# Kernel tuning notes

Hardware: AMD Instinct MI355X
Metric: run time of the kernel (lower is better)

Reference implementation:

```python
import jax, jax.numpy as jnp
import numpy as np

BINS = 10          # config.bins
SCOPE = 2          # config.dropout_scope_lowest (continue_train=True)
BASE_RATE = 0.0    # self.dropout_rate = zeros(1) when continue_train
THRESH = (BINS - SCOPE) / BINS   # edges[bins - dropout_scope]
UPPER = 1.0 + 1e-6               # edges[bins] (last edge += 1e-6)


def _forward(pred, target, rand_mat, hard_rand, pos_prop):
    B, C = pred.shape
    Bf = jnp.asarray(B, pred.dtype)
    # BCEWithLogits, reduction='none': logaddexp(0,x) - x*t
    bce = jnp.logaddexp(0.0, pred) - pred * target                     # [B,C]
    # g is detached in the torch code
    g = jax.lax.stop_gradient(jnp.abs(jax.nn.sigmoid(pred) - target))  # [B,C]
    # per-class loss -> normalized -> per-class dropout rate
    loss_c = bce.sum(0)                                                # [C]
    ln = jnp.log10(1.0 + loss_c)
    norm = 5.0 - 10.0 * (ln - ln.min()) / (ln.max() - ln.min())
    drate = jnp.maximum(jax.nn.sigmoid(norm), BASE_RATE)               # [C]
    # pos/neg balance bookkeeping (all per-class)
    pos_sum = target.sum(0)                                            # [C]
    neg_sum = Bf - pos_sum
    bal_pos = pos_prop * Bf
    bal_neg = Bf - bal_pos
    pos_gt = pos_sum > bal_pos                                         # majority is positives
    neg_gt = neg_sum > bal_neg                                         # majority is negatives
    balance_num = jnp.where(pos_gt, bal_pos, jnp.where(neg_gt, bal_neg, 0.0))
    dropout_num = jnp.floor(
        jnp.where(pos_gt, pos_sum - bal_pos,
                  jnp.where(neg_gt, neg_sum - bal_neg, 0.0))).astype(jnp.int32)
    # hard/easy class split: uniform(1,C) > dropout_rate
    hard = hard_rand[0] > drate                                        # [C] bool
    maj_lab = pos_gt.astype(pred.dtype)
    min_lab = neg_gt.astype(pred.dtype)
    is_maj = target == maj_lab[None, :]                                # [B,C]
    is_min = target == min_lab[None, :]
    maj_cnt = is_maj.sum(0).astype(pred.dtype)                         # [C]
    min_cnt = is_min.sum(0).astype(pred.dtype)
    # hard branch: reweight majority samples to balance_num/|majority|
    w_hard = jnp.where(is_maj, (balance_num / jnp.maximum(maj_cnt, 1.0))[None, :], 1.0)
    # easy branch: zero the dropout_num easiest (smallest g) majority samples,
    # rescale minority by (B - balance_num)/|minority|
    g_m = jnp.where(is_maj, g, jnp.inf)
    ranks = jnp.argsort(jnp.argsort(g_m, axis=0), axis=0)              # rank among majority by g asc
    drop_easy = is_maj & (ranks < dropout_num[None, :])
    w_easy = jnp.where(is_min & (min_cnt > 0)[None, :],
                       ((Bf - balance_num) / jnp.maximum(min_cnt, 1.0))[None, :], 1.0)
    w_easy = jnp.where(drop_easy, 0.0, w_easy)
    weights = jnp.where(hard[None, :], w_hard, w_easy)                 # [B,C]
    # random dropping of high-|g| (hard-gradient band) samples
    idxs = ((g >= THRESH) & (g < UPPER)).astype(pred.dtype)
    drop_idxs = (rand_mat > drate[None, :]).astype(pred.dtype)
    weights = weights * (1.0 - drop_idxs * idxs)
    return (bce * weights).mean()


def setup_inputs() -> dict:
    key = jax.random.key(0)
    k1, k2, k3, k4, k5 = jax.random.split(key, 5)
    B, C = 131072, 40
    pred = jax.random.normal(k1, (B, C), jnp.float32) * 2.0
    target = jax.random.bernoulli(k2, 0.5, (B, C)).astype(jnp.float32)
    rand_mat = jax.random.uniform(k3, (B, C), jnp.float32)
    hard_rand = jax.random.uniform(k4, (1, C), jnp.float32)
    pos_prop = jax.random.uniform(k5, (C,), jnp.float32, minval=0.3, maxval=0.7)
    return {"pred": pred, "target": target, "rand_mat": rand_mat,
            "hard_rand": hard_rand, "pos_prop": pos_prop}


def reference(pred, target, rand_mat, hard_rand, pos_prop):
    return _forward(pred, target, rand_mat, hard_rand, pos_prop)
```

## Files before the change

### kernel.cpp

```cpp
#include <hip/hip_runtime.h>
#include <hip/hip_bf16.h>
#include <math.h>
#include <stddef.h>

#define BN 131072
#define CN 40
#define NTOT (BN * CN)
#define MASKW (BN / 64)
#define NBLK 1024
#define NCHUNK 8
#define CROWS (BN / NCHUNK)

struct Ws {
    double acc;
    double pad0;
    unsigned ghist0[CN][4096];
    unsigned ghist1[CN][1024];
    unsigned ghist2[CN][256];
    double lossc[CN];
    int    posc[CN];
    float drate[CN];
    float majl[CN];
    float minl[CN];
    float w_hard[CN];
    float w_easy[CN];
    int   hardf[CN];
    int   kdrop[CN];
    int   minpos[CN];
    union {
        unsigned long long mask[CN][MASKW];
        struct { float lpart[CN][NBLK]; int ppart[CN][NBLK]; } parts;
    } u;
    unsigned long long eqmask[CN][MASKW];
    unsigned keys[CN][BN];
};

__device__ __forceinline__ float bce_f(float x, float t) {
    float m = fmaxf(x, 0.0f);
    return m + log1pf(expf(-fabsf(x))) - x * t;
}
__device__ __forceinline__ float g_f(float x, float t) {
    float s = 1.0f / (1.0f + expf(-x));
    return fabsf(s - t);
}
__device__ __forceinline__ void bce_g(float x, float t, float& bce, float& g) {
    float e   = expf(-fabsf(x));
    bce       = fmaxf(x, 0.0f) + log1pf(e) - x * t;
    float inv = 1.0f / (1.0f + e);
    float s   = (x >= 0.0f) ? inv : e * inv;
    g         = fabsf(s - t);
}
__device__ __forceinline__ unsigned masked_key(unsigned key, unsigned majb) {
    return ((key & 1u) == majb) ? (key >> 1) : 0xFFFFFFFFu;
}
__device__ __forceinline__ bool col_active(const Ws* ws, int c) {
    return (ws->kdrop[c] > 0) && (ws->hardf[c] == 0);
}

template<int PER, int NBINS>
__device__ __forceinline__ void scan_pick(const unsigned* __restrict__ gh,
                                          unsigned krem,
                                          unsigned* wsum ,
                                          unsigned* out2 ) {
    int tid = threadIdx.x, lane = tid & 63, w = tid >> 6;
    unsigned v[PER];
    unsigned s = 0;
    #pragma unroll
    for (int i = 0; i < PER; ++i) {
        int idx = tid * PER + i;
        v[i] = (idx < NBINS) ? gh[idx] : 0u;
        s += v[i];
    }
    unsigned isc = s;
    #pragma unroll
    for (int d = 1; d < 64; d <<= 1) {
        unsigned o = __shfl_up(isc, (unsigned)d, 64);
        if (lane >= d) isc += o;
    }
    if (lane == 63) wsum[w] = isc;
    __syncthreads();
    unsigned wpre = 0;
    #pragma unroll
    for (int j = 0; j < 16; ++j) wpre += (j < w) ? wsum[j] : 0u;
    unsigned inc = wpre + isc, prev = inc - s;
    if (prev < krem && inc >= krem) {
        unsigned cum = prev;
        #pragma unroll
        for (int i = 0; i < PER; ++i) {
            if (cum < krem && cum + v[i] >= krem) {
                out2[0] = (unsigned)(tid * PER + i);
                out2[1] = krem - cum;
            }
            cum += v[i];
        }
    }
    __syncthreads();
}

__global__ __launch_bounds__(640) void k_fuse(const float* __restrict__ pred,
                                              const float* __restrict__ tgt,
                                              Ws* __restrict__ ws) {
    __shared__ unsigned shk[128 * 41];
    __shared__ float sl[CN];
    __shared__ int   sp[CN];
    int tid = threadIdx.x;
    if (tid < CN) { sl[tid] = 0.0f; sp[tid] = 0; }
    __syncthreads();

    int  tile  = (blockIdx.x & 7) * 128 + (blockIdx.x >> 3);
    long tile0 = (long)tile * 5120;
    int  c0    = (tid * 4) % 40;
    float accl[4] = {0, 0, 0, 0};
    int   cntp[4] = {0, 0, 0, 0};

    #pragma unroll
    for (int j = 0; j < 2; ++j) {
        int e = j * 2560 + tid * 4;
        const float4 p = *(const float4*)(pred + tile0 + e);
        const float4 t = *(const float4*)(tgt + tile0 + e);
        int r = e / 40;
        #pragma unroll
        for (int u = 0; u < 4; ++u) {
            float pu = (&p.x)[u], tu = (&t.x)[u];
            float bce, g;
            bce_g(pu, tu, bce, g);
            accl[u] += bce;
            int tb = (tu != 0.0f) ? 1 : 0;
            cntp[u] += tb;
            shk[r * 41 + c0 + u] = (__float_as_uint(g) << 1) | (unsigned)tb;
        }
    }
    #pragma unroll
    for (int u = 0; u < 4; ++u) {
        atomicAdd(&sl[c0 + u], accl[u]);
        atomicAdd(&sp[c0 + u], cntp[u]);
    }
    __syncthreads();

    int w = tid / 128, r = tid % 128;
    int row0 = tile * 128;
    #pragma unroll
    for (int cc = 0; cc < 8; ++cc) {
        int c = w * 8 + cc;
        ws->keys[c][row0 + r] = shk[r * 41 + c];
    }
    if (tid < CN) {
        ws->u.parts.lpart[tid][blockIdx.x] = sl[tid];
        ws->u.parts.ppart[tid][blockIdx.x] = sp[tid];
    }
}

__global__ __launch_bounds__(1024) void k_params(const float* __restrict__ hard_rand,
                                                 const float* __restrict__ pos_prop,
                                                 Ws* __restrict__ ws, int use_part) {
    int tid = threadIdx.x;
    __shared__ double sred[CN][17];
    __shared__ int    spre[CN][17];
    __shared__ double lossv[CN];
    __shared__ int    posv[CN];
    __shared__ double lns[CN];
    __shared__ double smn, smx;
    if (use_part) {
        if (tid < CN * 16) {
            int c = tid >> 4, j = tid & 15;
            double s = 0.0; int p = 0;
            for (int i = j; i < NBLK; i += 16) {
                s += (double)ws->u.parts.lpart[c][i];
                p += ws->u.parts.ppart[c][i];
            }
            sred[c][j] = s; spre[c][j] = p;
        }
        __syncthreads();
        if (tid < CN) {
            double s = 0.0; int p = 0;
            for (int j = 0; j < 16; ++j) { s += sred[tid][j]; p += spre[tid][j]; }
            lossv[tid] = s; posv[tid] = p;
        }
    } else {
        if (tid < CN) { lossv[tid] = ws->lossc[tid]; posv[tid] = ws->posc[tid]; }
    }
    __syncthreads();
    if (tid < CN) lns[tid] = log10(1.0 + lossv[tid]);
    __syncthreads();
    if (tid == 0) {
        double a = lns[0], b = lns[0];
        for (int i = 1; i < CN; i++) { a = fmin(a, lns[i]); b = fmax(b, lns[i]); }
        smn = a; smx = b;
    }
    __syncthreads();
    if (tid < CN) {
        int c = tid;
        double norm = 5.0 - 10.0 * (lns[c] - smn) / (smx - smn);
        float drate = (float)(1.0 / (1.0 + exp(-norm)));
        float Bf = (float)BN;
        float pos_sum = (float)posv[c];
        float neg_sum = Bf - pos_sum;
        float bal_pos = pos_prop[c] * Bf;
        float bal_neg = Bf - bal_pos;
        bool pos_gt = pos_sum > bal_pos;
        bool neg_gt = neg_sum > bal_neg;
        float balance = pos_gt ? bal_pos : (neg_gt ? bal_neg : 0.0f);
        float dnum_f  = pos_gt ? (pos_sum - bal_pos)
                               : (neg_gt ? (neg_sum - bal_neg) : 0.0f);
        int   kdrop   = (int)floorf(dnum_f);
        float majl = pos_gt ? 1.0f : 0.0f;
        float minl = neg_gt ? 1.0f : 0.0f;
        float maj_cnt = (majl == 1.0f) ? pos_sum : neg_sum;
        float min_cnt = (minl == 1.0f) ? pos_sum : neg_sum;
        ws->drate[c]  = drate;
        ws->majl[c]   = majl;
        ws->minl[c]   = minl;
        ws->w_hard[c] = balance / fmaxf(maj_cnt, 1.0f);
        ws->w_easy[c] = (Bf - balance) / fmaxf(min_cnt, 1.0f);
        ws->hardf[c]  = (hard_rand[c] > drate) ? 1 : 0;
        ws->kdrop[c]  = kdrop;
        ws->minpos[c] = (min_cnt > 0.0f) ? 1 : 0;
    }
}

__global__ __launch_bounds__(1024) void k_hist0(Ws* __restrict__ ws) {
    int c = blockIdx.x >> 3, chunk = blockIdx.x & 7;
    if (!col_active(ws, c)) return;
    unsigned majb = (ws->majl[c] != 0.0f) ? 1u : 0u;
    const uint4* __restrict__ kc4 =
        (const uint4*)(ws->keys[c] + chunk * CROWS);
    __shared__ unsigned h[4096];
    int tid = threadIdx.x;
    for (int i = tid; i < 4096; i += 1024) h[i] = 0;
    __syncthreads();
    for (int b4 = tid; b4 < CROWS / 4; b4 += 1024) {
        uint4 kk = kc4[b4];
        unsigned ks[4] = {kk.x, kk.y, kk.z, kk.w};
        #pragma unroll
        for (int q = 0; q < 4; ++q)
            if ((ks[q] & 1u) == majb) atomicAdd(&h[(ks[q] >> 1) >> 18], 1u);
    }
    __syncthreads();
    for (int i = tid; i < 4096; i += 1024)
        if (h[i]) atomicAdd(&ws->ghist0[c][i], h[i]);
}

__global__ __launch_bounds__(1024) void k_hist1(Ws* __restrict__ ws) {
    int c = blockIdx.x >> 3, chunk = blockIdx.x & 7;
    if (!col_active(ws, c)) return;
    __shared__ unsigned wsum[16];
    __shared__ unsigned out2[2];
    scan_pick<4, 4096>(ws->ghist0[c], (unsigned)ws->kdrop[c], wsum, out2);
    unsigned p0 = out2[0];
    unsigned majb = (ws->majl[c] != 0.0f) ? 1u : 0u;
    const uint4* __restrict__ kc4 =
        (const uint4*)(ws->keys[c] + chunk * CROWS);
    __shared__ unsigned h[1024];
    int tid = threadIdx.x;
    h[tid] = 0;
    __syncthreads();
    for (int b4 = tid; b4 < CROWS / 4; b4 += 1024) {
        uint4 kk = kc4[b4];
        unsigned ks[4] = {kk.x, kk.y, kk.z, kk.w};
        #pragma unroll
        for (int q = 0; q < 4; ++q)
            if ((ks[q] & 1u) == majb) {
                unsigned mk = ks[q] >> 1;
                if ((mk >> 18) == p0) atomicAdd(&h[(mk >> 8) & 0x3FFu], 1u);
            }
    }
    __syncthreads();
    if (h[tid]) atomicAdd(&ws->ghist1[c][tid], h[tid]);
}

__global__ __launch_bounds__(1024) void k_hist2(Ws* __restrict__ ws) {
    int c = blockIdx.x >> 3, chunk = blockIdx.x & 7;
    if (!col_active(ws, c)) return;
    __shared__ unsigned wsum[16];
    __shared__ unsigned out2[2];
    scan_pick<4, 4096>(ws->ghist0[c], (unsigned)ws->kdrop[c], wsum, out2);
    unsigned p0 = out2[0], krem1 = out2[1];
    scan_pick<1, 1024>(ws->ghist1[c], krem1, wsum, out2);
    unsigned pp = (p0 << 10) | out2[0];
    unsigned majb = (ws->majl[c] != 0.0f) ? 1u : 0u;
    const uint4* __restrict__ kc4 =
        (const uint4*)(ws->keys[c] + chunk * CROWS);
    __shared__ unsigned h[256];
    int tid = threadIdx.x;
    if (tid < 256) h[tid] = 0;
    __syncthreads();
    for (int b4 = tid; b4 < CROWS / 4; b4 += 1024) {
        uint4 kk = kc4[b4];
        unsigned ks[4] = {kk.x, kk.y, kk.z, kk.w};
        #pragma unroll
        for (int q = 0; q < 4; ++q)
            if ((ks[q] & 1u) == majb) {
                unsigned mk = ks[q] >> 1;
                if ((mk >> 8) == pp) atomicAdd(&h[mk & 0xFFu], 1u);
            }
    }
    __syncthreads();
    if (tid < 256 && h[tid]) atomicAdd(&ws->ghist2[c][tid], h[tid]);
}

__global__ __launch_bounds__(1024) void k_mask(Ws* __restrict__ ws) {
    int c = blockIdx.x >> 3, chunk = blockIdx.x & 7;
    int tid = threadIdx.x;
    unsigned long long* mrow = ws->u.mask[c];
    if (!col_active(ws, c)) {
        if (tid < MASKW / NCHUNK) mrow[chunk * (MASKW / NCHUNK) + tid] = 0ull;
        return;
    }
    __shared__ unsigned wsum[16];
    __shared__ unsigned out2[2];
    scan_pick<4, 4096>(ws->ghist0[c], (unsigned)ws->kdrop[c], wsum, out2);
    unsigned p0 = out2[0], krem1 = out2[1];
    scan_pick<1, 1024>(ws->ghist1[c], krem1, wsum, out2);
    unsigned p1 = out2[0], krem2 = out2[1];
    scan_pick<1, 256>(ws->ghist2[c], krem2, wsum, out2);
    unsigned T = (p0 << 18) | (p1 << 8) | out2[0];

    unsigned majb = (ws->majl[c] != 0.0f) ? 1u : 0u;
    const unsigned* __restrict__ kc = ws->keys[c];
    unsigned long long* erow = ws->eqmask[c];
    int lane = tid & 63, w = tid >> 6;
    int base = chunk * CROWS;
    for (int it = 0; it < CROWS / 1024; ++it) {
        int b = base + it * 1024 + tid;
        unsigned m = masked_key(kc[b], majb);
        unsigned long long blt = __ballot(m < T);
        unsigned long long beq = __ballot(m == T);
        if (lane == 0) {
            int word = (base >> 6) + it * 16 + w;
            mrow[word] = blt;
            erow[word] = beq;
        }
    }
}

__global__ __launch_bounds__(1024) void k_tie(Ws* __restrict__ ws) {
    int c = blockIdx.x;
    if (!col_active(ws, c)) return;
    __shared__ unsigned wsum[16];
    __shared__ unsigned out2[2];
    scan_pick<4, 4096>(ws->ghist0[c], (unsigned)ws->kdrop[c], wsum, out2);
    unsigned krem1 = out2[1];
    scan_pick<1, 1024>(ws->ghist1[c], krem1, wsum, out2);
    unsigned krem2 = out2[1];
    scan_pick<1, 256>(ws->ghist2[c], krem2, wsum, out2);
    unsigned need = out2[1];

    int tid = threadIdx.x, lane = tid & 63, w = tid >> 6;
    const unsigned long long* erow = ws->eqmask[c];
    unsigned long long* mrow = ws->u.mask[c];
    unsigned long long e0 = erow[2 * tid], e1 = erow[2 * tid + 1];
    unsigned pc0 = (unsigned)__popcll(e0), pc1 = (unsigned)__popcll(e1);
    unsigned cnt = pc0 + pc1;
    unsigned isc = cnt;
    #pragma unroll
    for (int d = 1; d < 64; d <<= 1) {
        unsigned o = __shfl_up(isc, (unsigned)d, 64);
        if (lane >= d) isc += o;
    }
    if (lane == 63) wsum[w] = isc;
    __syncthreads();
    unsigned wpre = 0;
    #pragma unroll
    for (int j = 0; j < 16; ++j) wpre += (j < w) ? wsum[j] : 0u;
    unsigned prev = wpre + isc - cnt;

    #pragma unroll
    for (int half = 0; half < 2; ++half) {
        unsigned long long e = half ? e1 : e0;
        unsigned pc = half ? pc1 : pc0;
        unsigned p  = half ? prev + pc0 : prev;
        if (pc > 0 && p < need) {
            unsigned keep = need - p;
            if (keep > pc) keep = pc;
            unsigned long long sel;
            if (keep == pc) sel = e;
            else {
                sel = 0ull;
                unsigned long long m = e;
                for (unsigned i = 0; i < keep; ++i) {
                    unsigned long long lsb = m & (~m + 1ull);
                    sel |= lsb;
                    m ^= lsb;
                }
            }
            mrow[2 * tid + half] |= sel;
        }
    }
}

__global__ __launch_bounds__(640) void k_final2(const float* __restrict__ pred,
                                                const float* __restrict__ tgt,
                                                const float* __restrict__ rnd,
                                                Ws* __restrict__ ws) {
    int tid = threadIdx.x;
    long tile0 = (long)blockIdx.x * 5120;
    int  c0    = (tid * 4) % 40;
    float drate[4], majl[4], minl[4], wh[4], we[4];
    int hf[4], mp[4];
    #pragma unroll
    for (int u = 0; u < 4; ++u) {
        int c = c0 + u;
        drate[u] = ws->drate[c]; majl[u] = ws->majl[c]; minl[u] = ws->minl[c];
        wh[u] = ws->w_hard[c];   we[u] = ws->w_easy[c];
        hf[u] = ws->hardf[c];    mp[u] = ws->minpos[c];
    }
    double acc = 0.0;
    #pragma unroll
    for (int j = 0; j < 2; ++j) {
        long i = tile0 + j * 2560 + tid * 4;
        const float4 p  = *(const float4*)(pred + i);
        const float4 t  = *(const float4*)(tgt + i);
        const float4 rr = *(const float4*)(rnd + i);
        int b = (int)(i / 40);
        int wsh = b >> 6, bit = b & 63;
        #pragma unroll
        for (int u = 0; u < 4; ++u) {
            float pu = (&p.x)[u], tu = (&t.x)[u], ru = (&rr.x)[u];
            float bce, g;
            bce_g(pu, tu, bce, g);
            float w;
            if (hf[u]) {
                w = (tu == majl[u]) ? wh[u] : 1.0f;
            } else {
                bool dropped = (ws->u.mask[c0 + u][wsh] >> bit) & 1ull;
                w = dropped ? 0.0f : ((tu == minl[u] && mp[u]) ? we[u] : 1.0f);
            }
            if (g >= 0.8f && g < 1.000001f && ru > drate[u]) w = 0.0f;
            acc += (double)(bce * w);
        }
    }
    __shared__ double sd[640];
    sd[tid] = acc;
    __syncthreads();
    for (int s = 320; s >= 5; s >>= 1) {
        if (tid < s) sd[tid] += sd[tid + s];
        __syncthreads();
    }
    if (tid == 0) {
        double v = sd[0] + sd[1] + sd[2] + sd[3] + sd[4];
        atomicAdd(&ws->acc, v);
    }
}

__global__ void k_write(Ws* __restrict__ ws, float* __restrict__ out) {
    out[0] = (float)(ws->acc / (double)NTOT);
}

__global__ void k_colreduce(const float* __restrict__ pred,
                            const float* __restrict__ tgt,
                            Ws* __restrict__ ws) {
    __shared__ float sl[CN];
    __shared__ int   sp[CN];
    int tid = threadIdx.x;
    if (tid < CN) { sl[tid] = 0.0f; sp[tid] = 0; }
    __syncthreads();
    int stride = gridDim.x * blockDim.x;
    for (int i = blockIdx.x * blockDim.x + tid; i < NTOT; i += stride) {
        int c = i % CN;
        float p = pred[i], t = tgt[i];
        atomicAdd(&sl[c], bce_f(p, t));
        if (t != 0.0f) atomicAdd(&sp[c], 1);
    }
    __syncthreads();
    if (tid < CN) {
        atomicAdd(&ws->lossc[tid], (double)sl[tid]);
        atomicAdd(&ws->posc[tid], sp[tid]);
    }
}

__global__ __launch_bounds__(1024) void k_select(const float* __restrict__ pred,
                                                 const float* __restrict__ tgt,
                                                 Ws* __restrict__ ws) {
    int c   = blockIdx.x;
    int tid = threadIdx.x;
    int k   = ws->kdrop[c];
    bool easy = (ws->hardf[c] == 0);
    unsigned long long* mrow = ws->u.mask[c];
    if (k <= 0 || !easy) {
        for (int i = tid; i < MASKW; i += 1024) mrow[i] = 0ull;
        return;
    }
    float majl = ws->majl[c];
    __shared__ unsigned h[256];
    __shared__ unsigned cum[256];
    __shared__ unsigned sh_sel, sh_krem;
    unsigned prefix = 0;
    unsigned krem   = (unsigned)k;
    for (int level = 0; level < 4; ++level) {
        int shift = 24 - 8 * level;
        for (int i = tid; i < 256; i += 1024) h[i] = 0;
        __syncthreads();
        for (int b = tid; b < BN; b += 1024) {
            float t = tgt[b * CN + c];
            if (t == majl) {
                unsigned bits = __float_as_uint(g_f(pred[b * CN + c], t));
                bool ok = (level == 0) || ((bits >> (shift + 8)) == prefix);
                if (ok) atomicAdd(&h[(bits >> shift) & 0xFFu], 1u);
            }
        }
        __syncthreads();
        if (tid < 256) cum[tid] = h[tid];
        __syncthreads();
        for (int off = 1; off < 256; off <<= 1) {
            unsigned v = 0;
            if (tid < 256 && tid >= off) v = cum[tid - off];
            __syncthreads();
            if (tid < 256 && tid >= off) cum[tid] += v;
            __syncthreads();
        }
        if (tid < 256) {
            unsigned prev = (tid == 0) ? 0u : cum[tid - 1];
            if (cum[tid] >= krem && prev < krem) {
                sh_sel  = (unsigned)tid;
                sh_krem = krem - prev;
            }
        }
        __syncthreads();
        prefix = (prefix << 8) | sh_sel;
        krem   = sh_krem;
        __syncthreads();
    }
    unsigned T    = prefix;
    unsigned need = krem;
    __shared__ unsigned wcnt[16];
    unsigned base = 0;
    int lane = tid & 63, wid = tid >> 6;
    for (int chunk = 0; chunk < BN / 1024; ++chunk) {
        int b = chunk * 1024 + tid;
        float t = tgt[b * CN + c];
        bool ismaj = (t == majl);
        unsigned bits = 0xFFFFFFFFu;
        if (ismaj) bits = __float_as_uint(g_f(pred[b * CN + c], t));
        bool lt = ismaj && (bits < T);
        bool eq = ismaj && (bits == T);
        unsigned long long bal = __ballot(eq);
        if (lane == 0) wcnt[wid] = (unsigned)__popcll(bal);
        __syncthreads();
        unsigned woff = 0, tot = 0;
        for (int w = 0; w < 16; ++w) {
            unsigned v = wcnt[w];
            if (w < wid) woff += v;
            tot += v;
        }
        unsigned long long lanemask = (lane == 0) ? 0ull : ((~0ull) >> (64 - lane));
        unsigned myrank = base + woff + (unsigned)__popcll(bal & lanemask);
        bool dropped = lt || (eq && myrank < need);
        unsigned long long bd = __ballot(dropped);
        if (lane == 0) mrow[chunk * 16 + wid] = bd;
        base += tot;
        __syncthreads();
    }
}

__global__ void k_final(const float* __restrict__ pred,
                        const float* __restrict__ tgt,
                        const float* __restrict__ rnd,
                        Ws* __restrict__ ws) {
    __shared__ double sdata[256];
    double acc = 0.0;
    int stride = gridDim.x * blockDim.x;
    for (int i = blockIdx.x * blockDim.x + threadIdx.x; i < NTOT; i += stride) {
        int b = i / CN;
        int c = i - b * CN;
        float p = pred[i], t = tgt[i], r = rnd[i];
        float bce = bce_f(p, t);
        float g   = g_f(p, t);
        float w;
        if (ws->hardf[c]) {
            w = (t == ws->majl[c]) ? ws->w_hard[c] : 1.0f;
        } else {
            bool dropped = (ws->u.mask[c][b >> 6] >> (b & 63)) & 1ull;
            if (dropped) w = 0.0f;
            else w = ((t == ws->minl[c]) && ws->minpos[c]) ? ws->w_easy[c] : 1.0f;
        }
        if ((g >= 0.8f) && (g < 1.000001f) && (r > ws->drate[c])) w = 0.0f;
        acc += (double)(bce * w);
    }
    sdata[threadIdx.x] = acc;
    __syncthreads();
    for (int s = blockDim.x / 2; s > 0; s >>= 1) {
        if (threadIdx.x < s) sdata[threadIdx.x] += sdata[threadIdx.x + s];
        __syncthreads();
    }
    if (threadIdx.x == 0) atomicAdd(&ws->acc, sdata[0]);
}

extern "C" void kernel_launch(void* const* d_in, const int* in_sizes, int n_in,
                              void* d_out, int out_size, void* d_ws, size_t ws_size,
                              hipStream_t stream) {
    const float* pred      = (const float*)d_in[0];
    const float* tgt       = (const float*)d_in[1];
    const float* rnd       = (const float*)d_in[2];
    const float* hard_rand = (const float*)d_in[3];
    const float* pos_prop  = (const float*)d_in[4];
    Ws* ws = (Ws*)d_ws;

    if (ws_size >= sizeof(Ws)) {
        hipMemsetAsync(d_ws, 0, offsetof(Ws, lossc), stream);
        k_fuse  <<<NBLK, 640, 0, stream>>>(pred, tgt, ws);
        k_params<<<1, 1024, 0, stream>>>(hard_rand, pos_prop, ws, 1);
        k_hist0 <<<CN * NCHUNK, 1024, 0, stream>>>(ws);
        k_hist1 <<<CN * NCHUNK, 1024, 0, stream>>>(ws);
        k_hist2 <<<CN * NCHUNK, 1024, 0, stream>>>(ws);
        k_mask  <<<CN * NCHUNK, 1024, 0, stream>>>(ws);
        k_tie   <<<CN, 1024, 0, stream>>>(ws);
        k_final2<<<NBLK, 640, 0, stream>>>(pred, tgt, rnd, ws);
    } else {
        hipMemsetAsync(d_ws, 0, offsetof(Ws, drate), stream);
        k_colreduce<<<2048, 256, 0, stream>>>(pred, tgt, ws);
        k_params<<<1, 1024, 0, stream>>>(hard_rand, pos_prop, ws, 0);
        k_select<<<CN, 1024, 0, stream>>>(pred, tgt, ws);
        k_final <<<2048, 256, 0, stream>>>(pred, tgt, rnd, ws);
    }
    k_write<<<1, 1, 0, stream>>>(ws, (float*)d_out);
}
```

Baseline: 209.2 us.

## Fuse param computation into first histogram pass and fold final write into reduce

```diff
diff --git a/kernel.cpp b/kernel.cpp
--- a/kernel.cpp
+++ b/kernel.cpp
@@ -13,7 +13,8 @@
 
 struct Ws {
     double acc;
-    double pad0;
+    unsigned done;
+    unsigned pad0;
     unsigned ghist0[CN][4096];
     unsigned ghist1[CN][1024];
     unsigned ghist2[CN][256];
@@ -36,17 +37,19 @@
 };
 
 __device__ __forceinline__ float bce_f(float x, float t) {
-    float m = fmaxf(x, 0.0f);
-    return m + log1pf(expf(-fabsf(x))) - x * t;
+    float e = __expf(-fabsf(x));
+    return fmaxf(x, 0.0f) + __logf(1.0f + e) - x * t;
 }
 __device__ __forceinline__ float g_f(float x, float t) {
-    float s = 1.0f / (1.0f + expf(-x));
+    float e   = __expf(-fabsf(x));
+    float inv = __builtin_amdgcn_rcpf(1.0f + e);
+    float s   = (x >= 0.0f) ? inv : e * inv;
     return fabsf(s - t);
 }
 __device__ __forceinline__ void bce_g(float x, float t, float& bce, float& g) {
-    float e   = expf(-fabsf(x));
-    bce       = fmaxf(x, 0.0f) + log1pf(e) - x * t;
-    float inv = 1.0f / (1.0f + e);
+    float e   = __expf(-fabsf(x));
+    bce       = fmaxf(x, 0.0f) + __logf(1.0f + e) - x * t;
+    float inv = __builtin_amdgcn_rcpf(1.0f + e);
     float s   = (x >= 0.0f) ? inv : e * inv;
     g         = fabsf(s - t);
 }
@@ -150,37 +153,324 @@
     }
 }
 
+__global__ __launch_bounds__(1024) void k_sel0(const float* __restrict__ hard_rand,
+                                               const float* __restrict__ pos_prop,
+                                               Ws* __restrict__ ws) {
+    const int bid = blockIdx.x;
+    const int c = bid >> 3, chunk = bid & 7;
+    const int tid = threadIdx.x, lane = tid & 63, wv = tid >> 6;
+
+    __shared__ unsigned h[4096];
+    __shared__ double s_lns[CN];
+    __shared__ int s_pos;
+    __shared__ int s_active, s_kdrop;
+    __shared__ unsigned s_majb;
+
+    for (int j = wv; j < CN; j += 16) {
+        double s = 0.0;
+        for (int q = lane; q < NBLK; q += 64)
+            s += (double)ws->u.parts.lpart[j][q];
+        #pragma unroll
+        for (int d = 32; d >= 1; d >>= 1) s += __shfl_down(s, d, 64);
+        if (lane == 0) s_lns[j] = log10(1.0 + s);
+    }
+    if (wv == 15) {
+        int p = 0;
+        for (int q = lane; q < NBLK; q += 64) p += ws->u.parts.ppart[c][q];
+        #pragma unroll
+        for (int d = 32; d >= 1; d >>= 1) p += __shfl_down(p, d, 64);
+        if (lane == 0) s_pos = p;
+    }
+    __syncthreads();
+    if (tid == 0) {
+        double mn = s_lns[0], mx = s_lns[0];
+        for (int i = 1; i < CN; ++i) { mn = fmin(mn, s_lns[i]); mx = fmax(mx, s_lns[i]); }
+        double norm = 5.0 - 10.0 * (s_lns[c] - mn) / (mx - mn);
+        float drate = (float)(1.0 / (1.0 + exp(-norm)));
+        float Bf = (float)BN;
+        float pos_sum = (float)s_pos;
+        float neg_sum = Bf - pos_sum;
+        float bal_pos = pos_prop[c] * Bf;
+        float bal_neg = Bf - bal_pos;
+        bool pos_gt = pos_sum > bal_pos;
+        bool neg_gt = neg_sum > bal_neg;
+        float balance = pos_gt ? bal_pos : (neg_gt ? bal_neg : 0.0f);
+        float dnum_f  = pos_gt ? (pos_sum - bal_pos)
+                               : (neg_gt ? (neg_sum - bal_neg) : 0.0f);
+        int   kdrop   = (int)floorf(dnum_f);
+        float majl = pos_gt ? 1.0f : 0.0f;
+        float minl = neg_gt ? 1.0f : 0.0f;
+        float maj_cnt = (majl == 1.0f) ? pos_sum : neg_sum;
+        float min_cnt = (minl == 1.0f) ? pos_sum : neg_sum;
+        int hardf = (hard_rand[c] > drate) ? 1 : 0;
+        if (chunk == 0) {
+            ws->drate[c]  = drate;
+            ws->majl[c]   = majl;
+            ws->minl[c]   = minl;
+            ws->w_hard[c] = balance / fmaxf(maj_cnt, 1.0f);
+            ws->w_easy[c] = (Bf - balance) / fmaxf(min_cnt, 1.0f);
+            ws->hardf[c]  = hardf;
+            ws->kdrop[c]  = kdrop;
+            ws->minpos[c] = (min_cnt > 0.0f) ? 1 : 0;
+        }
+        s_active = (kdrop > 0 && hardf == 0) ? 1 : 0;
+        s_kdrop  = kdrop;
+        s_majb   = (majl != 0.0f) ? 1u : 0u;
+    }
+    __syncthreads();
+    if (!s_active) return;
+    const unsigned majb = s_majb;
+    const uint4* kc4 = (const uint4*)(ws->keys[c] + chunk * CROWS);
+
+    for (int i = tid; i < 4096; i += 1024) h[i] = 0;
+    __syncthreads();
+    for (int b4 = tid; b4 < CROWS / 4; b4 += 1024) {
+        uint4 kk = kc4[b4];
+        unsigned ks[4] = {kk.x, kk.y, kk.z, kk.w};
+        #pragma unroll
+        for (int q = 0; q < 4; ++q)
+            if ((ks[q] & 1u) == majb) atomicAdd(&h[(ks[q] >> 1) >> 18], 1u);
+    }
+    __syncthreads();
+    for (int i = tid; i < 4096; i += 1024)
+        if (h[i]) atomicAdd(&ws->ghist0[c][i], h[i]);
+}
+
+__global__ __launch_bounds__(1024) void k_hist1(Ws* __restrict__ ws) {
+    int c = blockIdx.x >> 3, chunk = blockIdx.x & 7;
+    if (!col_active(ws, c)) return;
+    __shared__ unsigned wsum[16];
+    __shared__ unsigned out2[2];
+    scan_pick<4, 4096>(ws->ghist0[c], (unsigned)ws->kdrop[c], wsum, out2);
+    unsigned p0 = out2[0];
+    unsigned majb = (ws->majl[c] != 0.0f) ? 1u : 0u;
+    const uint4* __restrict__ kc4 = (const uint4*)(ws->keys[c] + chunk * CROWS);
+    __shared__ unsigned h[1024];
+    int tid = threadIdx.x;
+    h[tid] = 0;
+    __syncthreads();
+    for (int b4 = tid; b4 < CROWS / 4; b4 += 1024) {
+        uint4 kk = kc4[b4];
+        unsigned ks[4] = {kk.x, kk.y, kk.z, kk.w};
+        #pragma unroll
+        for (int q = 0; q < 4; ++q)
+            if ((ks[q] & 1u) == majb) {
+                unsigned mk = ks[q] >> 1;
+                if ((mk >> 18) == p0) atomicAdd(&h[(mk >> 8) & 0x3FFu], 1u);
+            }
+    }
+    __syncthreads();
+    if (h[tid]) atomicAdd(&ws->ghist1[c][tid], h[tid]);
+}
+
+__global__ __launch_bounds__(1024) void k_hist2(Ws* __restrict__ ws) {
+    int c = blockIdx.x >> 3, chunk = blockIdx.x & 7;
+    if (!col_active(ws, c)) return;
+    __shared__ unsigned wsum[16];
+    __shared__ unsigned out2[2];
+    scan_pick<4, 4096>(ws->ghist0[c], (unsigned)ws->kdrop[c], wsum, out2);
+    unsigned p0 = out2[0], krem1 = out2[1];
+    scan_pick<1, 1024>(ws->ghist1[c], krem1, wsum, out2);
+    unsigned pp = (p0 << 10) | out2[0];
+    unsigned majb = (ws->majl[c] != 0.0f) ? 1u : 0u;
+    const uint4* __restrict__ kc4 = (const uint4*)(ws->keys[c] + chunk * CROWS);
+    __shared__ unsigned h[256];
+    int tid = threadIdx.x;
+    if (tid < 256) h[tid] = 0;
+    __syncthreads();
+    for (int b4 = tid; b4 < CROWS / 4; b4 += 1024) {
+        uint4 kk = kc4[b4];
+        unsigned ks[4] = {kk.x, kk.y, kk.z, kk.w};
+        #pragma unroll
+        for (int q = 0; q < 4; ++q)
+            if ((ks[q] & 1u) == majb) {
+                unsigned mk = ks[q] >> 1;
+                if ((mk >> 8) == pp) atomicAdd(&h[mk & 0xFFu], 1u);
+            }
+    }
+    __syncthreads();
+    if (tid < 256 && h[tid]) atomicAdd(&ws->ghist2[c][tid], h[tid]);
+}
+
+__global__ __launch_bounds__(1024) void k_mask(Ws* __restrict__ ws) {
+    int c = blockIdx.x >> 3, chunk = blockIdx.x & 7;
+    int tid = threadIdx.x;
+    unsigned long long* mrow = ws->u.mask[c];
+    if (!col_active(ws, c)) {
+        if (tid < MASKW / NCHUNK) mrow[chunk * (MASKW / NCHUNK) + tid] = 0ull;
+        return;
+    }
+    __shared__ unsigned wsum[16];
+    __shared__ unsigned out2[2];
+    scan_pick<4, 4096>(ws->ghist0[c], (unsigned)ws->kdrop[c], wsum, out2);
+    unsigned p0 = out2[0], krem1 = out2[1];
+    scan_pick<1, 1024>(ws->ghist1[c], krem1, wsum, out2);
+    unsigned p1 = out2[0], krem2 = out2[1];
+    scan_pick<1, 256>(ws->ghist2[c], krem2, wsum, out2);
+    unsigned T = (p0 << 18) | (p1 << 8) | out2[0];
+
+    unsigned majb = (ws->majl[c] != 0.0f) ? 1u : 0u;
+    const unsigned* __restrict__ kc = ws->keys[c];
+    unsigned long long* erow = ws->eqmask[c];
+    int lane = tid & 63, w = tid >> 6;
+    int base = chunk * CROWS;
+    for (int it = 0; it < CROWS / 1024; ++it) {
+        int b = base + it * 1024 + tid;
+        unsigned m = masked_key(kc[b], majb);
+        unsigned long long blt = __ballot(m < T);
+        unsigned long long beq = __ballot(m == T);
+        if (lane == 0) {
+            int word = (base >> 6) + it * 16 + w;
+            mrow[word] = blt;
+            erow[word] = beq;
+        }
+    }
+}
+
+__global__ __launch_bounds__(1024) void k_tie(Ws* __restrict__ ws) {
+    int c = blockIdx.x;
+    if (!col_active(ws, c)) return;
+    __shared__ unsigned wsum[16];
+    __shared__ unsigned out2[2];
+    scan_pick<4, 4096>(ws->ghist0[c], (unsigned)ws->kdrop[c], wsum, out2);
+    unsigned krem1 = out2[1];
+    scan_pick<1, 1024>(ws->ghist1[c], krem1, wsum, out2);
+    unsigned krem2 = out2[1];
+    scan_pick<1, 256>(ws->ghist2[c], krem2, wsum, out2);
+    unsigned need = out2[1];
+
+    int tid = threadIdx.x, lane = tid & 63, w = tid >> 6;
+    const unsigned long long* erow = ws->eqmask[c];
+    unsigned long long* mrow = ws->u.mask[c];
+    unsigned long long e0 = erow[2 * tid], e1 = erow[2 * tid + 1];
+    unsigned pc0 = (unsigned)__popcll(e0), pc1 = (unsigned)__popcll(e1);
+    unsigned cnt = pc0 + pc1;
+    unsigned isc = cnt;
+    #pragma unroll
+    for (int d = 1; d < 64; d <<= 1) {
+        unsigned o = __shfl_up(isc, (unsigned)d, 64);
+        if (lane >= d) isc += o;
+    }
+    if (lane == 63) wsum[w] = isc;
+    __syncthreads();
+    unsigned wpre = 0;
+    #pragma unroll
+    for (int j = 0; j < 16; ++j) wpre += (j < w) ? wsum[j] : 0u;
+    unsigned prev = wpre + isc - cnt;
+    #pragma unroll
+    for (int half = 0; half < 2; ++half) {
+        unsigned long long e = half ? e1 : e0;
+        unsigned pc = half ? pc1 : pc0;
+        unsigned p  = half ? prev + pc0 : prev;
+        if (pc > 0 && p < need) {
+            unsigned keep = need - p;
+            if (keep > pc) keep = pc;
+            unsigned long long sel;
+            if (keep == pc) sel = e;
+            else {
+                sel = 0ull;
+                unsigned long long m = e;
+                for (unsigned i = 0; i < keep; ++i) {
+                    unsigned long long lsb = m & (~m + 1ull);
+                    sel |= lsb;
+                    m ^= lsb;
+                }
+            }
+            mrow[2 * tid + half] |= sel;
+        }
+    }
+}
+
+__global__ __launch_bounds__(640) void k_final3(const float* __restrict__ pred,
+                                                const float* __restrict__ tgt,
+                                                const float* __restrict__ rnd,
+                                                Ws* __restrict__ ws,
+                                                float* __restrict__ out) {
+    int tid = threadIdx.x;
+    long tile0 = (long)blockIdx.x * 5120;
+    int  c0    = (tid * 4) % 40;
+    float drate[4], majl[4], minl[4], wh[4], we[4];
+    int hf[4], mp[4];
+    #pragma unroll
+    for (int u = 0; u < 4; ++u) {
+        int c = c0 + u;
+        drate[u] = ws->drate[c]; majl[u] = ws->majl[c]; minl[u] = ws->minl[c];
+        wh[u] = ws->w_hard[c];   we[u] = ws->w_easy[c];
+        hf[u] = ws->hardf[c];    mp[u] = ws->minpos[c];
+    }
+    double acc = 0.0;
+    #pragma unroll
+    for (int j = 0; j < 2; ++j) {
+        long i = tile0 + j * 2560 + tid * 4;
+        const float4 p  = *(const float4*)(pred + i);
+        const float4 t  = *(const float4*)(tgt + i);
+        const float4 rr = *(const float4*)(rnd + i);
+        int b = (int)(i / 40);
+        int wsh = b >> 6, bit = b & 63;
+        #pragma unroll
+        for (int u = 0; u < 4; ++u) {
+            float pu = (&p.x)[u], tu = (&t.x)[u], ru = (&rr.x)[u];
+            float bce, g;
+            bce_g(pu, tu, bce, g);
+            float w;
+            if (hf[u]) {
+                w = (tu == majl[u]) ? wh[u] : 1.0f;
+            } else {
+                bool dropped = (ws->u.mask[c0 + u][wsh] >> bit) & 1ull;
+                w = dropped ? 0.0f : ((tu == minl[u] && mp[u]) ? we[u] : 1.0f);
+            }
+            if (g >= 0.8f && g < 1.000001f && ru > drate[u]) w = 0.0f;
+            acc += (double)(bce * w);
+        }
+    }
+    __shared__ double sd[640];
+    sd[tid] = acc;
+    __syncthreads();
+    for (int s = 320; s >= 5; s >>= 1) {
+        if (tid < s) sd[tid] += sd[tid + s];
+        __syncthreads();
+    }
+    if (tid == 0) {
+        double v = sd[0] + sd[1] + sd[2] + sd[3] + sd[4];
+        atomicAdd(&ws->acc, v);
+        __threadfence();
+        unsigned t = atomicAdd(&ws->done, 1u);
+        if (t == (unsigned)(NBLK - 1)) {
+            double total = atomicAdd(&ws->acc, 0.0);
+            out[0] = (float)(total / (double)NTOT);
+        }
+    }
+}
+
+__global__ void k_colreduce(const float* __restrict__ pred,
+                            const float* __restrict__ tgt,
+                            Ws* __restrict__ ws) {
+    __shared__ float sl[CN];
+    __shared__ int   sp[CN];
+    int tid = threadIdx.x;
+    if (tid < CN) { sl[tid] = 0.0f; sp[tid] = 0; }
+    __syncthreads();
+    int stride = gridDim.x * blockDim.x;
+    for (int i = blockIdx.x * blockDim.x + tid; i < NTOT; i += stride) {
+        int c = i % CN;
+        float p = pred[i], t = tgt[i];
+        atomicAdd(&sl[c], bce_f(p, t));
+        if (t != 0.0f) atomicAdd(&sp[c], 1);
+    }
+    __syncthreads();
+    if (tid < CN) {
+        atomicAdd(&ws->lossc[tid], (double)sl[tid]);
+        atomicAdd(&ws->posc[tid], sp[tid]);
+    }
+}
+
 __global__ __launch_bounds__(1024) void k_params(const float* __restrict__ hard_rand,
                                                  const float* __restrict__ pos_prop,
-                                                 Ws* __restrict__ ws, int use_part) {
-    int tid = threadIdx.x;
-    __shared__ double sred[CN][17];
-    __shared__ int    spre[CN][17];
-    __shared__ double lossv[CN];
-    __shared__ int    posv[CN];
+                                                 Ws* __restrict__ ws) {
+    int tid = threadIdx.x;
     __shared__ double lns[CN];
     __shared__ double smn, smx;
-    if (use_part) {
-        if (tid < CN * 16) {
-            int c = tid >> 4, j = tid & 15;
-            double s = 0.0; int p = 0;
-            for (int i = j; i < NBLK; i += 16) {
-                s += (double)ws->u.parts.lpart[c][i];
-                p += ws->u.parts.ppart[c][i];
-            }
-            sred[c][j] = s; spre[c][j] = p;
-        }
-        __syncthreads();
-        if (tid < CN) {
-            double s = 0.0; int p = 0;
-            for (int j = 0; j < 16; ++j) { s += sred[tid][j]; p += spre[tid][j]; }
-            lossv[tid] = s; posv[tid] = p;
-        }
-    } else {
-        if (tid < CN) { lossv[tid] = ws->lossc[tid]; posv[tid] = ws->posc[tid]; }
-    }
-    __syncthreads();
-    if (tid < CN) lns[tid] = log10(1.0 + lossv[tid]);
+    if (tid < CN) lns[tid] = log10(1.0 + ws->lossc[tid]);
     __syncthreads();
     if (tid == 0) {
         double a = lns[0], b = lns[0];
@@ -193,7 +483,7 @@
         double norm = 5.0 - 10.0 * (lns[c] - smn) / (smx - smn);
         float drate = (float)(1.0 / (1.0 + exp(-norm)));
         float Bf = (float)BN;
-        float pos_sum = (float)posv[c];
+        float pos_sum = (float)ws->posc[c];
         float neg_sum = Bf - pos_sum;
         float bal_pos = pos_prop[c] * Bf;
         float bal_neg = Bf - bal_pos;
@@ -218,256 +508,6 @@
     }
 }
 
-__global__ __launch_bounds__(1024) void k_hist0(Ws* __restrict__ ws) {
-    int c = blockIdx.x >> 3, chunk = blockIdx.x & 7;
-    if (!col_active(ws, c)) return;
-    unsigned majb = (ws->majl[c] != 0.0f) ? 1u : 0u;
-    const uint4* __restrict__ kc4 =
-        (const uint4*)(ws->keys[c] + chunk * CROWS);
-    __shared__ unsigned h[4096];
-    int tid = threadIdx.x;
-    for (int i = tid; i < 4096; i += 1024) h[i] = 0;
-    __syncthreads();
-    for (int b4 = tid; b4 < CROWS / 4; b4 += 1024) {
-        uint4 kk = kc4[b4];
-        unsigned ks[4] = {kk.x, kk.y, kk.z, kk.w};
-        #pragma unroll
-        for (int q = 0; q < 4; ++q)
-            if ((ks[q] & 1u) == majb) atomicAdd(&h[(ks[q] >> 1) >> 18], 1u);
-    }
-    __syncthreads();
-    for (int i = tid; i < 4096; i += 1024)
-        if (h[i]) atomicAdd(&ws->ghist0[c][i], h[i]);
-}
-
-__global__ __launch_bounds__(1024) void k_hist1(Ws* __restrict__ ws) {
-    int c = blockIdx.x >> 3, chunk = blockIdx.x & 7;
-    if (!col_active(ws, c)) return;
-    __shared__ unsigned wsum[16];
-    __shared__ unsigned out2[2];
-    scan_pick<4, 4096>(ws->ghist0[c], (unsigned)ws->kdrop[c], wsum, out2);
-    unsigned p0 = out2[0];
-    unsigned majb = (ws->majl[c] != 0.0f) ? 1u : 0u;
-    const uint4* __restrict__ kc4 =
-        (const uint4*)(ws->keys[c] + chunk * CROWS);
-    __shared__ unsigned h[1024];
-    int tid = threadIdx.x;
-    h[tid] = 0;
-    __syncthreads();
-    for (int b4 = tid; b4 < CROWS / 4; b4 += 1024) {
-        uint4 kk = kc4[b4];
-        unsigned ks[4] = {kk.x, kk.y, kk.z, kk.w};
-        #pragma unroll
-        for (int q = 0; q < 4; ++q)
-            if ((ks[q] & 1u) == majb) {
-                unsigned mk = ks[q] >> 1;
-                if ((mk >> 18) == p0) atomicAdd(&h[(mk >> 8) & 0x3FFu], 1u);
-            }
-    }
-    __syncthreads();
-    if (h[tid]) atomicAdd(&ws->ghist1[c][tid], h[tid]);
-}
-
-__global__ __launch_bounds__(1024) void k_hist2(Ws* __restrict__ ws) {
-    int c = blockIdx.x >> 3, chunk = blockIdx.x & 7;
-    if (!col_active(ws, c)) return;
-    __shared__ unsigned wsum[16];
-    __shared__ unsigned out2[2];
-    scan_pick<4, 4096>(ws->ghist0[c], (unsigned)ws->kdrop[c], wsum, out2);
-    unsigned p0 = out2[0], krem1 = out2[1];
-    scan_pick<1, 1024>(ws->ghist1[c], krem1, wsum, out2);
-    unsigned pp = (p0 << 10) | out2[0];
-    unsigned majb = (ws->majl[c] != 0.0f) ? 1u : 0u;
-    const uint4* __restrict__ kc4 =
-        (const uint4*)(ws->keys[c] + chunk * CROWS);
-    __shared__ unsigned h[256];
-    int tid = threadIdx.x;
-    if (tid < 256) h[tid] = 0;
-    __syncthreads();
-    for (int b4 = tid; b4 < CROWS / 4; b4 += 1024) {
-        uint4 kk = kc4[b4];
-        unsigned ks[4] = {kk.x, kk.y, kk.z, kk.w};
-        #pragma unroll
-        for (int q = 0; q < 4; ++q)
-            if ((ks[q] & 1u) == majb) {
-                unsigned mk = ks[q] >> 1;
-                if ((mk >> 8) == pp) atomicAdd(&h[mk & 0xFFu], 1u);
-            }
-    }
-    __syncthreads();
-    if (tid < 256 && h[tid]) atomicAdd(&ws->ghist2[c][tid], h[tid]);
-}
-
-__global__ __launch_bounds__(1024) void k_mask(Ws* __restrict__ ws) {
-    int c = blockIdx.x >> 3, chunk = blockIdx.x & 7;
-    int tid = threadIdx.x;
-    unsigned long long* mrow = ws->u.mask[c];
-    if (!col_active(ws, c)) {
-        if (tid < MASKW / NCHUNK) mrow[chunk * (MASKW / NCHUNK) + tid] = 0ull;
-        return;
-    }
-    __shared__ unsigned wsum[16];
-    __shared__ unsigned out2[2];
-    scan_pick<4, 4096>(ws->ghist0[c], (unsigned)ws->kdrop[c], wsum, out2);
-    unsigned p0 = out2[0], krem1 = out2[1];
-    scan_pick<1, 1024>(ws->ghist1[c], krem1, wsum, out2);
-    unsigned p1 = out2[0], krem2 = out2[1];
-    scan_pick<1, 256>(ws->ghist2[c], krem2, wsum, out2);
-    unsigned T = (p0 << 18) | (p1 << 8) | out2[0];
-
-    unsigned majb = (ws->majl[c] != 0.0f) ? 1u : 0u;
-    const unsigned* __restrict__ kc = ws->keys[c];
-    unsigned long long* erow = ws->eqmask[c];
-    int lane = tid & 63, w = tid >> 6;
-    int base = chunk * CROWS;
-    for (int it = 0; it < CROWS / 1024; ++it) {
-        int b = base + it * 1024 + tid;
-        unsigned m = masked_key(kc[b], majb);
-        unsigned long long blt = __ballot(m < T);
-        unsigned long long beq = __ballot(m == T);
-        if (lane == 0) {
-            int word = (base >> 6) + it * 16 + w;
-            mrow[word] = blt;
-            erow[word] = beq;
-        }
-    }
-}
-
-__global__ __launch_bounds__(1024) void k_tie(Ws* __restrict__ ws) {
-    int c = blockIdx.x;
-    if (!col_active(ws, c)) return;
-    __shared__ unsigned wsum[16];
-    __shared__ unsigned out2[2];
-    scan_pick<4, 4096>(ws->ghist0[c], (unsigned)ws->kdrop[c], wsum, out2);
-    unsigned krem1 = out2[1];
-    scan_pick<1, 1024>(ws->ghist1[c], krem1, wsum, out2);
-    unsigned krem2 = out2[1];
-    scan_pick<1, 256>(ws->ghist2[c], krem2, wsum, out2);
-    unsigned need = out2[1];
-
-    int tid = threadIdx.x, lane = tid & 63, w = tid >> 6;
-    const unsigned long long* erow = ws->eqmask[c];
-    unsigned long long* mrow = ws->u.mask[c];
-    unsigned long long e0 = erow[2 * tid], e1 = erow[2 * tid + 1];
-    unsigned pc0 = (unsigned)__popcll(e0), pc1 = (unsigned)__popcll(e1);
-    unsigned cnt = pc0 + pc1;
-    unsigned isc = cnt;
-    #pragma unroll
-    for (int d = 1; d < 64; d <<= 1) {
-        unsigned o = __shfl_up(isc, (unsigned)d, 64);
-        if (lane >= d) isc += o;
-    }
-    if (lane == 63) wsum[w] = isc;
-    __syncthreads();
-    unsigned wpre = 0;
-    #pragma unroll
-    for (int j = 0; j < 16; ++j) wpre += (j < w) ? wsum[j] : 0u;
-    unsigned prev = wpre + isc - cnt;
-
-    #pragma unroll
-    for (int half = 0; half < 2; ++half) {
-        unsigned long long e = half ? e1 : e0;
-        unsigned pc = half ? pc1 : pc0;
-        unsigned p  = half ? prev + pc0 : prev;
-        if (pc > 0 && p < need) {
-            unsigned keep = need - p;
-            if (keep > pc) keep = pc;
-            unsigned long long sel;
-            if (keep == pc) sel = e;
-            else {
-                sel = 0ull;
-                unsigned long long m = e;
-                for (unsigned i = 0; i < keep; ++i) {
-                    unsigned long long lsb = m & (~m + 1ull);
-                    sel |= lsb;
-                    m ^= lsb;
-                }
-            }
-            mrow[2 * tid + half] |= sel;
-        }
-    }
-}
-
-__global__ __launch_bounds__(640) void k_final2(const float* __restrict__ pred,
-                                                const float* __restrict__ tgt,
-                                                const float* __restrict__ rnd,
-                                                Ws* __restrict__ ws) {
-    int tid = threadIdx.x;
-    long tile0 = (long)blockIdx.x * 5120;
-    int  c0    = (tid * 4) % 40;
-    float drate[4], majl[4], minl[4], wh[4], we[4];
-    int hf[4], mp[4];
-    #pragma unroll
-    for (int u = 0; u < 4; ++u) {
-        int c = c0 + u;
-        drate[u] = ws->drate[c]; majl[u] = ws->majl[c]; minl[u] = ws->minl[c];
-        wh[u] = ws->w_hard[c];   we[u] = ws->w_easy[c];
-        hf[u] = ws->hardf[c];    mp[u] = ws->minpos[c];
-    }
-    double acc = 0.0;
-    #pragma unroll
-    for (int j = 0; j < 2; ++j) {
-        long i = tile0 + j * 2560 + tid * 4;
-        const float4 p  = *(const float4*)(pred + i);
-        const float4 t  = *(const float4*)(tgt + i);
-        const float4 rr = *(const float4*)(rnd + i);
-        int b = (int)(i / 40);
-        int wsh = b >> 6, bit = b & 63;
-        #pragma unroll
-        for (int u = 0; u < 4; ++u) {
-            float pu = (&p.x)[u], tu = (&t.x)[u], ru = (&rr.x)[u];
-            float bce, g;
-            bce_g(pu, tu, bce, g);
-            float w;
-            if (hf[u]) {
-                w = (tu == majl[u]) ? wh[u] : 1.0f;
-            } else {
-                bool dropped = (ws->u.mask[c0 + u][wsh] >> bit) & 1ull;
-                w = dropped ? 0.0f : ((tu == minl[u] && mp[u]) ? we[u] : 1.0f);
-            }
-            if (g >= 0.8f && g < 1.000001f && ru > drate[u]) w = 0.0f;
-            acc += (double)(bce * w);
-        }
-    }
-    __shared__ double sd[640];
-    sd[tid] = acc;
-    __syncthreads();
-    for (int s = 320; s >= 5; s >>= 1) {
-        if (tid < s) sd[tid] += sd[tid + s];
-        __syncthreads();
-    }
-    if (tid == 0) {
-        double v = sd[0] + sd[1] + sd[2] + sd[3] + sd[4];
-        atomicAdd(&ws->acc, v);
-    }
-}
-
-__global__ void k_write(Ws* __restrict__ ws, float* __restrict__ out) {
-    out[0] = (float)(ws->acc / (double)NTOT);
-}
-
-__global__ void k_colreduce(const float* __restrict__ pred,
-                            const float* __restrict__ tgt,
-                            Ws* __restrict__ ws) {
-    __shared__ float sl[CN];
-    __shared__ int   sp[CN];
-    int tid = threadIdx.x;
-    if (tid < CN) { sl[tid] = 0.0f; sp[tid] = 0; }
-    __syncthreads();
-    int stride = gridDim.x * blockDim.x;
-    for (int i = blockIdx.x * blockDim.x + tid; i < NTOT; i += stride) {
-        int c = i % CN;
-        float p = pred[i], t = tgt[i];
-        atomicAdd(&sl[c], bce_f(p, t));
-        if (t != 0.0f) atomicAdd(&sp[c], 1);
-    }
-    __syncthreads();
-    if (tid < CN) {
-        atomicAdd(&ws->lossc[tid], (double)sl[tid]);
-        atomicAdd(&ws->posc[tid], sp[tid]);
-    }
-}
-
 __global__ __launch_bounds__(1024) void k_select(const float* __restrict__ pred,
                                                  const float* __restrict__ tgt,
                                                  Ws* __restrict__ ws) {
@@ -585,6 +625,10 @@
     if (threadIdx.x == 0) atomicAdd(&ws->acc, sdata[0]);
 }
 
+__global__ void k_write(Ws* __restrict__ ws, float* __restrict__ out) {
+    out[0] = (float)(ws->acc / (double)NTOT);
+}
+
 extern "C" void kernel_launch(void* const* d_in, const int* in_sizes, int n_in,
                               void* d_out, int out_size, void* d_ws, size_t ws_size,
                               hipStream_t stream) {
@@ -598,19 +642,18 @@
     if (ws_size >= sizeof(Ws)) {
         hipMemsetAsync(d_ws, 0, offsetof(Ws, lossc), stream);
         k_fuse  <<<NBLK, 640, 0, stream>>>(pred, tgt, ws);
-        k_params<<<1, 1024, 0, stream>>>(hard_rand, pos_prop, ws, 1);
-        k_hist0 <<<CN * NCHUNK, 1024, 0, stream>>>(ws);
+        k_sel0  <<<CN * NCHUNK, 1024, 0, stream>>>(hard_rand, pos_prop, ws);
         k_hist1 <<<CN * NCHUNK, 1024, 0, stream>>>(ws);
         k_hist2 <<<CN * NCHUNK, 1024, 0, stream>>>(ws);
         k_mask  <<<CN * NCHUNK, 1024, 0, stream>>>(ws);
         k_tie   <<<CN, 1024, 0, stream>>>(ws);
-        k_final2<<<NBLK, 640, 0, stream>>>(pred, tgt, rnd, ws);
+        k_final3<<<NBLK, 640, 0, stream>>>(pred, tgt, rnd, ws, (float*)d_out);
     } else {
         hipMemsetAsync(d_ws, 0, offsetof(Ws, drate), stream);
         k_colreduce<<<2048, 256, 0, stream>>>(pred, tgt, ws);
-        k_params<<<1, 1024, 0, stream>>>(hard_rand, pos_prop, ws, 0);
+        k_params<<<1, 1024, 0, stream>>>(hard_rand, pos_prop, ws);
         k_select<<<CN, 1024, 0, stream>>>(pred, tgt, ws);
         k_final <<<2048, 256, 0, stream>>>(pred, tgt, rnd, ws);
-    }
-    k_write<<<1, 1, 0, stream>>>(ws, (float*)d_out);
-}
+        k_write <<<1, 1, 0, stream>>>(ws, (float*)d_out);
+    }
+}
```

Result: faster. 202.0 us (-3.5%).
